# Kernel tuning notes

Hardware: AMD Instinct MI355X
Metric: run time of the kernel (lower is better)

The kernel has to match this reference:

```python
import jax, jax.numpy as jnp
import numpy as np

B, T, D, U = 64, 1024, 300, 300


def setup_inputs() -> dict:
    key = jax.random.key(0)
    ks = jax.random.split(key, 12)
    inputs = jax.random.normal(ks[0], (B, T, D), jnp.float32)
    lengths = jax.random.randint(ks[1], (B,), T // 2, T + 1)
    mask = jnp.arange(T)[None, :] < lengths[:, None]  # [B,T] bool

    def w(k, shape, fan_in):
        return jax.random.normal(k, shape, jnp.float32) * (1.0 / np.sqrt(fan_in))

    # Keras GRU (reset_after=True): kernel [D,3U], recurrent_kernel [U,3U], bias [2,3U]
    k_fwd = w(ks[2], (D, 3 * U), D)
    rk_fwd = w(ks[3], (U, 3 * U), U)
    b_fwd = jnp.zeros((2, 3 * U), jnp.float32)
    k_bwd = w(ks[4], (D, 3 * U), D)
    rk_bwd = w(ks[5], (U, 3 * U), U)
    b_bwd = jnp.zeros((2, 3 * U), jnp.float32)
    w_fc = w(ks[6], (2 * U, U), 2 * U)
    b_fc = jnp.zeros((U,), jnp.float32)
    return {
        "inputs": inputs, "mask": mask,
        "k_fwd": k_fwd, "rk_fwd": rk_fwd, "b_fwd": b_fwd,
        "k_bwd": k_bwd, "rk_bwd": rk_bwd, "b_bwd": b_bwd,
        "w_fc": w_fc, "b_fc": b_fc, "training": 0,
    }


def _gru_dir(x, mask, kernel, rkernel, bias):
    """Keras GRU v2 (reset_after=True), zero_output_for_mask, state frozen on masked steps.
    x: [B,T,D], mask: [B,T] bool -> (ys [B,T,U], h_final [B,U])"""
    b_in, b_rec = bias[0], bias[1]
    u = rkernel.shape[0]
    # precompute input projections for all timesteps (cuDNN-style hoisting)
    xp = jnp.einsum('btd,dk->btk', x, kernel) + b_in  # [B,T,3U]

    def step(h, inp):
        xt, mt = inp  # xt: [B,3U], mt: [B]
        rp = h @ rkernel + b_rec  # [B,3U]
        xz, xr, xh = jnp.split(xt, 3, axis=-1)
        rz, rr, rh = jnp.split(rp, 3, axis=-1)
        z = jax.nn.sigmoid(xz + rz)
        r = jax.nn.sigmoid(xr + rr)
        hh = jnp.tanh(xh + r * rh)
        h_new = z * h + (1.0 - z) * hh
        m = mt[:, None]
        h_carry = jnp.where(m, h_new, h)       # state does not update on masked steps
        y = jnp.where(m, h_new, jnp.zeros_like(h_new))  # zero_output_for_mask
        return h_carry, y

    h0 = jnp.zeros((x.shape[0], u), x.dtype)
    h_final, ys = jax.lax.scan(step, h0, (xp.transpose(1, 0, 2), mask.T))
    return ys.transpose(1, 0, 2), h_final


def reference(inputs, mask, k_fwd, rk_fwd, b_fwd, k_bwd, rk_bwd, b_bwd, w_fc, b_fc, training):
    mask = mask.astype(bool)
    x = inputs  # Dropout is identity at inference (training=0)
    y_f, h_f = _gru_dir(x, mask, k_fwd, rk_fwd, b_fwd)
    # backward direction: process reversed sequence/mask, then re-reverse outputs
    y_b, h_b = _gru_dir(x[:, ::-1], mask[:, ::-1], k_bwd, rk_bwd, b_bwd)
    y_b = y_b[:, ::-1]
    output = jnp.concatenate([y_f, y_b], axis=-1)  # [B,T,2U]
    state = jax.nn.relu(jnp.concatenate([h_f, h_b], axis=-1) @ w_fc + b_fc)  # [B,U]
    return output, state
```

## Files before the change

### kernel.cpp

```cpp
#include <hip/hip_runtime.h>
#include <hip/hip_bf16.h>


#define B_   64
#define T_   1024
#define D_   300
#define U_   300
#define NU   900
#define KP   320
#define NP   960
#define XPW  912
#define KB_  10
#define KRES 2
#define HSP  328
#define FRAGS_PER_DIR 570
#define NRESF 114
#define NWGM 4

typedef short short8 __attribute__((ext_vector_type(8)));
typedef float floatx4 __attribute__((ext_vector_type(4)));

__device__ __forceinline__ float b2f_bits(unsigned short u) {
  union { unsigned int i; float f; } v; v.i = ((unsigned int)u) << 16; return v.f;
}
__device__ __forceinline__ unsigned short f2b(float f) {
  __hip_bfloat16 h = __float2bfloat16(f);
  return *reinterpret_cast<unsigned short*>(&h);
}
__device__ __forceinline__ float sigm_f(float x) {
  float e = __expf(-x);
  return __fdividef(1.f, 1.f + e);
}
__device__ __forceinline__ float tanh_f(float x) {
  float e = __expf(2.f * x);
  return 1.f - __fdividef(2.f, e + 1.f);
}

__global__ __launch_bounds__(64) void k_detect(const unsigned int* __restrict__ xw,
                                               const unsigned char* __restrict__ mb,
                                               int* __restrict__ flags) {
  __shared__ int red[64];
  int tid = threadIdx.x;
  int hits = 0;
  for (int i = tid; i < 2048; i += 64) {
    unsigned int lo = xw[i] & 0xFFFFu;
    int e = (int)((lo >> 7) & 0xFF);
    if (e >= 105 && e <= 135) hits++;
  }
  red[tid] = hits;
  __syncthreads();
  if (tid == 0) {
    int s = 0;
    for (int i = 0; i < 64; ++i) s += red[i];
    flags[0] = (s >= 1024) ? 1 : 0;
    unsigned char b0 = mb[0], b1 = mb[1];
    flags[1] = (b1 == 0) ? 0 : ((b0 == 1 && b1 == 1) ? 1 : 2);
  }
}

__global__ __launch_bounds__(256) void k_lengths(const unsigned char* __restrict__ mraw,
                                                 const int* __restrict__ flags,
                                                 int* __restrict__ lens) {
  __shared__ int red[256];
  int b = blockIdx.x, tid = threadIdx.x;
  int mt = flags[1];
  int s = 0;
  if (mt == 0) {
    const int* m = (const int*)mraw;
    for (int t = tid; t < T_; t += 256) s += m[(size_t)b * T_ + t] ? 1 : 0;
  } else if (mt == 1) {
    for (int t = tid; t < T_; t += 256) s += mraw[(size_t)b * T_ + t] ? 1 : 0;
  } else {
    const unsigned short* m = (const unsigned short*)mraw;
    for (int t = tid; t < T_; t += 256) s += m[(size_t)b * T_ + t] ? 1 : 0;
  }
  red[tid] = s; __syncthreads();
  for (int off = 128; off > 0; off >>= 1) {
    if (tid < off) red[tid] += red[tid + off];
    __syncthreads();
  }
  if (tid == 0) lens[b] = red[0];
}

__global__ __launch_bounds__(256) void k_xpad(const void* __restrict__ xraw,
                                              const int* __restrict__ flags,
                                              unsigned short* __restrict__ xp) {
  int id = blockIdx.x * 256 + threadIdx.x;
  int row = id / 40, seg = id % 40;
  int kbase = seg * 8;
  int bf = flags[0];
  unsigned short v[8];
  if (bf) {
    const unsigned short* x = (const unsigned short*)xraw;
#pragma unroll
    for (int i = 0; i < 8; ++i) {
      int k = kbase + i;
      v[i] = (k < D_) ? x[(size_t)row * D_ + k] : (unsigned short)0;
    }
  } else {
    const float* x = (const float*)xraw;
#pragma unroll
    for (int i = 0; i < 8; ++i) {
      int k = kbase + i;
      v[i] = (k < D_) ? f2b(x[(size_t)row * D_ + k]) : (unsigned short)0;
    }
  }
  uint4 o;
  o.x = (unsigned)v[0] | ((unsigned)v[1] << 16);
  o.y = (unsigned)v[2] | ((unsigned)v[3] << 16);
  o.z = (unsigned)v[4] | ((unsigned)v[5] << 16);
  o.w = (unsigned)v[6] | ((unsigned)v[7] << 16);
  *(uint4*)(xp + (size_t)row * KP + kbase) = o;
}

__global__ __launch_bounds__(256) void k_wpad(const void* __restrict__ kf,
                                              const void* __restrict__ kb,
                                              const int* __restrict__ flags,
                                              unsigned short* __restrict__ kp) {
  int id = blockIdx.x * 256 + threadIdx.x;
  if (id >= 2 * KP * NP) return;
  int dir = id / (KP * NP);
  int r = id % (KP * NP);
  int k = r / NP, n = r % NP;
  int bf = flags[0];
  unsigned short v = 0;
  if (k < D_ && n < NU) {
    size_t si = (size_t)k * NU + n;
    if (bf) v = ((const unsigned short*)(dir ? kb : kf))[si];
    else    v = f2b(((const float*)(dir ? kb : kf))[si]);
  }
  kp[id] = v;
}

__global__ __launch_bounds__(256) void k_prep(const void* __restrict__ rkf,
                                              const void* __restrict__ rkb,
                                              const void* __restrict__ bfw,
                                              const void* __restrict__ bbw,
                                              const void* __restrict__ wfc,
                                              const void* __restrict__ bfc,
                                              const int* __restrict__ flags,
                                              unsigned short* __restrict__ rkc,
                                              float* __restrict__ biasc,
                                              unsigned short* __restrict__ wfcc,
                                              float* __restrict__ bfcc) {
  int i = blockIdx.x * 256 + threadIdx.x;
  int bf = flags[0];
  if (i < 2 * D_ * NU) {
    int dir = i / (D_ * NU), r = i % (D_ * NU);
    const void* src = dir ? rkb : rkf;
    rkc[i] = bf ? ((const unsigned short*)src)[r] : f2b(((const float*)src)[r]);
  }
  if (i < 2 * 2 * NU) {
    int dir = i / (2 * NU), r = i % (2 * NU);
    const void* src = dir ? bbw : bfw;
    biasc[i] = bf ? b2f_bits(((const unsigned short*)src)[r]) : ((const float*)src)[r];
  }
  if (i < 2 * U_ * U_) {
    wfcc[i] = bf ? ((const unsigned short*)wfc)[i] : f2b(((const float*)wfc)[i]);
  }
  if (i < U_) {
    bfcc[i] = bf ? b2f_bits(((const unsigned short*)bfc)[i]) : ((const float*)bfc)[i];
  }
}

__global__ __launch_bounds__(256) void k_bpack(const unsigned short* __restrict__ rkc,
                                               unsigned short* __restrict__ bpack) {
  int idx = blockIdx.x * 256 + threadIdx.x;
  const int total = 2 * FRAGS_PER_DIR * 512;
  if (idx >= total) return;
  int rem = idx;
  int j = rem & 7; rem >>= 3;
  int lane = rem & 63; rem >>= 6;
  int f = rem % FRAGS_PER_DIR;
  int dir = rem / FRAGS_PER_DIR;
  int w, fr, ntc;
  if (f < 180) { w = f / 60; fr = f - w * 60; ntc = 6; }
  else { int f2 = f - 180; w = 3 + f2 / 30; fr = f2 % 30; ntc = 3; }
  int kb = fr / ntc, nt = fr % ntc;
  int lb = nt / 3, g = nt % 3;
  int ub0 = (w < 3) ? 2 * w : 6 + (w - 3);
  int l15 = lane & 15, quad = lane >> 4;
  int k = kb * 32 + quad * 8 + j;
  int u = (ub0 + lb) * 16 + l15;
  unsigned short v = 0;
  if (k < U_ && u < U_) {
    v = rkc[(size_t)dir * U_ * NU + (size_t)k * NU + (size_t)g * U_ + u];
  }
  bpack[idx] = v;
}

template <bool XPF32>
__global__ __launch_bounds__(256) void k_gemm(const unsigned short* __restrict__ xpad,
                                              const unsigned short* __restrict__ kpad,
                                              const float* __restrict__ biasc,
                                              void* __restrict__ xp_out) {
  __shared__ __align__(16) unsigned short As[64 * 40];
  __shared__ __align__(16) unsigned short Bs[64 * 40];
  int tid = threadIdx.x;
  int wave = tid >> 6, lane = tid & 63;
  int m0 = blockIdx.x * 64, n0 = blockIdx.y * 64;
  int dir = blockIdx.z;
  const unsigned short* Bsrc = kpad + (size_t)dir * KP * NP;
  const float* bin = biasc + (size_t)dir * 2 * NU;

  floatx4 acc[4];
#pragma unroll
  for (int i = 0; i < 4; ++i) acc[i] = {0.f, 0.f, 0.f, 0.f};

  int arow = tid >> 2, aseg = tid & 3;
  int bk = tid & 31, bn8 = (tid >> 5) * 8;
  int fr = lane & 15, fq = lane >> 4;

  for (int kc = 0; kc < KP; kc += 32) {
    uint4 av = *(const uint4*)(xpad + (size_t)(m0 + arow) * KP + kc + aseg * 8);
    uint4 bv = *(const uint4*)(Bsrc + (size_t)(kc + bk) * NP + n0 + bn8);
    *(uint4*)(As + arow * 40 + aseg * 8) = av;
    unsigned short tmp[8];
    tmp[0] = bv.x & 0xffff; tmp[1] = bv.x >> 16;
    tmp[2] = bv.y & 0xffff; tmp[3] = bv.y >> 16;
    tmp[4] = bv.z & 0xffff; tmp[5] = bv.z >> 16;
    tmp[6] = bv.w & 0xffff; tmp[7] = bv.w >> 16;
#pragma unroll
    for (int i = 0; i < 8; ++i) Bs[(bn8 + i) * 40 + bk] = tmp[i];
    __syncthreads();
    short8 a = *(const short8*)(As + (wave * 16 + fr) * 40 + fq * 8);
#pragma unroll
    for (int nt = 0; nt < 4; ++nt) {
      short8 bfrag = *(const short8*)(Bs + (nt * 16 + fr) * 40 + fq * 8);
      acc[nt] = __builtin_amdgcn_mfma_f32_16x16x32_bf16(a, bfrag, acc[nt], 0, 0, 0);
    }
    __syncthreads();
  }
#pragma unroll
  for (int nt = 0; nt < 4; ++nt) {
    int col = n0 + nt * 16 + fr;
    if (col >= XPW) continue;
    float bi = (col < NU) ? bin[col] : 0.f;
#pragma unroll
    for (int r = 0; r < 4; ++r) {
      int m = m0 + wave * 16 + fq * 4 + r;
      float v = acc[nt][r] + bi;
      size_t idx = ((size_t)dir * 65536 + m) * XPW + col;
      if (XPF32) ((float*)xp_out)[idx] = v;
      else ((unsigned short*)xp_out)[idx] = f2b(v);
    }
  }
}

template <int NB, bool XPF32>
__device__ __forceinline__ void scan_loop(
    const unsigned short* __restrict__ bp,
    const unsigned short* __restrict__ sBw,
    unsigned short (*sHiP)[16][HSP],
    unsigned short (*sLoP)[16][HSP],
    const void* __restrict__ xp_all,
    unsigned short* __restrict__ out16, float* __restrict__ out32, int obf,
    const float* __restrict__ brec, const int* __restrict__ lens,
    float* __restrict__ hfin,
    int dir, int mg, int ub0, int l15, int quad) {
  constexpr int NTC = NB * 3;

  int ucl[NB]; bool cv[NB];
  float bz[NB], brg[NB], bh[NB];
#pragma unroll
  for (int lb = 0; lb < NB; ++lb) {
    int u = (ub0 + lb) * 16 + l15;
    bool v = (u < U_);
    cv[lb] = v;
    ucl[lb] = v ? u : 0;
    bz[lb] = brec[ucl[lb]]; brg[lb] = brec[U_ + ucl[lb]]; bh[lb] = brec[2 * U_ + ucl[lb]];
  }
  size_t xbase[4];
#pragma unroll
  for (int r = 0; r < 4; ++r)
    xbase[r] = ((size_t)dir * 65536 + (size_t)(mg * 16 + quad * 4 + r) * T_) * XPW;
  int mylen[4];
#pragma unroll
  for (int r = 0; r < 4; ++r) mylen[r] = lens[mg * 16 + quad * 4 + r];
  float hold[NB][4];
#pragma unroll
  for (int lb = 0; lb < NB; ++lb)
#pragma unroll
    for (int r = 0; r < 4; ++r) hold[lb][r] = 0.f;

#pragma unroll 1
  for (int s = 0; s < T_; ++s) {
    const int t = dir ? (T_ - 1 - s) : s;
    const int par = s & 1;
    const unsigned short (*hH)[HSP] = sHiP[par];
    const unsigned short (*hL)[HSP] = sLoP[par];

    floatx4 acc[NTC];
#pragma unroll
    for (int i = 0; i < NTC; ++i) acc[i] = {0.f, 0.f, 0.f, 0.f};

    short8 bA[NTC];
#pragma unroll
    for (int nt = 0; nt < NTC; ++nt)
      bA[nt] = *(const short8*)(bp + ((size_t)(KRES * NTC + nt)) * 512);
    short8 bB[NB == 1 ? NTC : 1];
    if constexpr (NB == 1) {
#pragma unroll
      for (int nt = 0; nt < NTC; ++nt)
        bB[nt] = *(const short8*)(bp + ((size_t)((KRES + 1) * NTC + nt)) * 512);
    }

    float X[NB][3][4];
#pragma unroll
    for (int r = 0; r < 4; ++r) {
      size_t ro = xbase[r] + (size_t)t * XPW;
      if (XPF32) {
        const float* xr = (const float*)xp_all + ro;
#pragma unroll
        for (int lb = 0; lb < NB; ++lb) {
          X[lb][0][r] = xr[ucl[lb]];
          X[lb][1][r] = xr[U_ + ucl[lb]];
          X[lb][2][r] = xr[2 * U_ + ucl[lb]];
        }
      } else {
        const unsigned short* xr = (const unsigned short*)xp_all + ro;
#pragma unroll
        for (int lb = 0; lb < NB; ++lb) {
          X[lb][0][r] = b2f_bits(xr[ucl[lb]]);
          X[lb][1][r] = b2f_bits(xr[U_ + ucl[lb]]);
          X[lb][2][r] = b2f_bits(xr[2 * U_ + ucl[lb]]);
        }
      }
    }

#pragma unroll
    for (int kb = 0; kb < KRES; ++kb) {
      short8 ah = *(const short8*)&hH[l15][kb * 32 + quad * 8];
      short8 al = *(const short8*)&hL[l15][kb * 32 + quad * 8];
#pragma unroll
      for (int nt = 0; nt < NTC; ++nt) {
        short8 b = *(const short8*)(sBw + ((size_t)(kb * NTC + nt)) * 512);
        acc[nt] = __builtin_amdgcn_mfma_f32_16x16x32_bf16(ah, b, acc[nt], 0, 0, 0);
      }
#pragma unroll
      for (int nt = 0; nt < NTC; ++nt) {
        short8 b = *(const short8*)(sBw + ((size_t)(kb * NTC + nt)) * 512);
        acc[nt] = __builtin_amdgcn_mfma_f32_16x16x32_bf16(al, b, acc[nt], 0, 0, 0);
      }
    }

    if constexpr (NB == 1) {
#pragma unroll
      for (int kb = KRES; kb < KB_; kb += 2) {
        {
          short8 ah = *(const short8*)&hH[l15][kb * 32 + quad * 8];
          short8 al = *(const short8*)&hL[l15][kb * 32 + quad * 8];
#pragma unroll
          for (int nt = 0; nt < NTC; ++nt)
            acc[nt] = __builtin_amdgcn_mfma_f32_16x16x32_bf16(ah, bA[nt], acc[nt], 0, 0, 0);
#pragma unroll
          for (int nt = 0; nt < NTC; ++nt)
            acc[nt] = __builtin_amdgcn_mfma_f32_16x16x32_bf16(al, bA[nt], acc[nt], 0, 0, 0);
          if (kb + 2 < KB_) {
#pragma unroll
            for (int nt = 0; nt < NTC; ++nt)
              bA[nt] = *(const short8*)(bp + ((size_t)((kb + 2) * NTC + nt)) * 512);
          }
        }
        {
          short8 ah = *(const short8*)&hH[l15][(kb + 1) * 32 + quad * 8];
          short8 al = *(const short8*)&hL[l15][(kb + 1) * 32 + quad * 8];
#pragma unroll
          for (int nt = 0; nt < NTC; ++nt)
            acc[nt] = __builtin_amdgcn_mfma_f32_16x16x32_bf16(ah, bB[nt], acc[nt], 0, 0, 0);
#pragma unroll
          for (int nt = 0; nt < NTC; ++nt)
            acc[nt] = __builtin_amdgcn_mfma_f32_16x16x32_bf16(al, bB[nt], acc[nt], 0, 0, 0);
          if (kb + 3 < KB_) {
#pragma unroll
            for (int nt = 0; nt < NTC; ++nt)
              bB[nt] = *(const short8*)(bp + ((size_t)((kb + 3) * NTC + nt)) * 512);
          }
        }
      }
    } else {
#pragma unroll
      for (int kb = KRES; kb < KB_; ++kb) {
        short8 ah = *(const short8*)&hH[l15][kb * 32 + quad * 8];
        short8 al = *(const short8*)&hL[l15][kb * 32 + quad * 8];
#pragma unroll
        for (int nt = 0; nt < NTC; ++nt)
          acc[nt] = __builtin_amdgcn_mfma_f32_16x16x32_bf16(ah, bA[nt], acc[nt], 0, 0, 0);
#pragma unroll
        for (int nt = 0; nt < NTC; ++nt)
          acc[nt] = __builtin_amdgcn_mfma_f32_16x16x32_bf16(al, bA[nt], acc[nt], 0, 0, 0);
        if (kb + 1 < KB_) {
#pragma unroll
          for (int nt = 0; nt < NTC; ++nt)
            bA[nt] = *(const short8*)(bp + ((size_t)((kb + 1) * NTC + nt)) * 512);
        }
      }
    }

    unsigned short (*nHi)[HSP] = sHiP[par ^ 1];
    unsigned short (*nLo)[HSP] = sLoP[par ^ 1];
#pragma unroll
    for (int r = 0; r < 4; ++r) {
      const int row = quad * 4 + r;
      const bool m = (t < mylen[r]);
      const size_t ob = ((size_t)(mg * 16 + row) * T_ + t) * 600 + (size_t)dir * U_;
#pragma unroll
      for (int lb = 0; lb < NB; ++lb) {
        float z  = sigm_f(X[lb][0][r] + acc[lb * 3 + 0][r] + bz[lb]);
        float rg = sigm_f(X[lb][1][r] + acc[lb * 3 + 1][r] + brg[lb]);
        float hh = tanh_f(X[lb][2][r] + rg * (acc[lb * 3 + 2][r] + bh[lb]));
        float hn = z * hold[lb][r] + (1.f - z) * hh;
        float hw = m ? hn : hold[lb][r];
        hold[lb][r] = hw;
        if (cv[lb]) {
          float y = m ? hn : 0.f;
          if (obf) out16[ob + ucl[lb]] = f2b(y); else out32[ob + ucl[lb]] = y;
          unsigned short hib = f2b(hw);
          nHi[row][ucl[lb]] = hib;
          nLo[row][ucl[lb]] = f2b(hw - b2f_bits(hib));
        }
      }
    }

    asm volatile("s_waitcnt lgkmcnt(0)" ::: "memory");
    __builtin_amdgcn_s_barrier();
  }

#pragma unroll
  for (int lb = 0; lb < NB; ++lb) {
    if (!cv[lb]) continue;
#pragma unroll
    for (int r = 0; r < 4; ++r)
      hfin[((size_t)dir * B_ + mg * 16 + quad * 4 + r) * 304 + ucl[lb]] = hold[lb][r];
  }
}

template <bool XPF32>
__global__ __launch_bounds__(1024, 1) void k_scan(const unsigned short* __restrict__ bpack,
                                                  const float* __restrict__ biasc,
                                                  const void* __restrict__ xp_all,
                                                  const int* __restrict__ lens,
                                                  const int* __restrict__ flags,
                                                  float* __restrict__ hfin,
                                                  void* __restrict__ outraw) {
  __shared__ unsigned short sHi[2][16][HSP];
  __shared__ unsigned short sLo[2][16][HSP];
  __shared__ __align__(16) unsigned short sB[NRESF * 512];

  const int tid = threadIdx.x;
  const int mg = blockIdx.x;
  const int dir = blockIdx.y;
  const int wave = tid >> 6, lane = tid & 63;
  const int l15 = lane & 15, quad = lane >> 4;
  const int obf = flags[0];
  unsigned short* out16 = (unsigned short*)outraw;
  float* out32 = (float*)outraw;

  const int NBLK = (wave < 3) ? 2 : 1;
  const int NTCw = NBLK * 3;
  const int UB0w = (wave < 3) ? 2 * wave : 6 + (wave - 3);
  const int FB   = (wave < 3) ? wave * 60 : 180 + (wave - 3) * 30;
  const int RB   = (wave < 3) ? wave * 12 : 36 + (wave - 3) * 6;

  {
    unsigned int* p0 = (unsigned int*)&sHi[0][0][0];
    unsigned int* p1 = (unsigned int*)&sLo[0][0][0];
    for (int i = tid; i < 2 * 16 * HSP / 2; i += 1024) { p0[i] = 0u; p1[i] = 0u; }
  }
  {
    const unsigned short* src = bpack + ((size_t)dir * FRAGS_PER_DIR + FB) * 512 + lane * 8;
    unsigned short* dst = sB + (size_t)RB * 512 + lane * 8;
    for (int j = 0; j < KRES * NTCw; ++j)
      *(uint4*)(dst + (size_t)j * 512) = *(const uint4*)(src + (size_t)j * 512);
  }
  __syncthreads();

  const unsigned short* bp = bpack + ((size_t)dir * FRAGS_PER_DIR + FB) * 512 + (size_t)lane * 8;
  const unsigned short* sBw = sB + (size_t)RB * 512 + (size_t)lane * 8;
  const float* brec = biasc + (size_t)dir * 2 * NU + NU;

  if (wave < 3)
    scan_loop<2, XPF32>(bp, sBw, sHi, sLo, xp_all, out16, out32, obf, brec, lens,
                        hfin, dir, mg, UB0w, l15, quad);
  else
    scan_loop<1, XPF32>(bp, sBw, sHi, sLo, xp_all, out16, out32, obf, brec, lens,
                        hfin, dir, mg, UB0w, l15, quad);
}

__global__ __launch_bounds__(320) void k_state(const float* __restrict__ hfin,
                                               const unsigned short* __restrict__ wfcc,
                                               const float* __restrict__ bfcc,
                                               const int* __restrict__ flags,
                                               void* __restrict__ outraw) {
  int b = blockIdx.x, u = threadIdx.x;
  if (u >= U_) return;
  int obf = flags[0];
  float acc = bfcc[u];
  const float* hf = hfin + (size_t)b * 304;
  const float* hb = hfin + ((size_t)B_ + b) * 304;
  for (int k = 0; k < U_; ++k) acc = fmaf(hf[k], b2f_bits(wfcc[(size_t)k * U_ + u]), acc);
  for (int k = 0; k < U_; ++k) acc = fmaf(hb[k], b2f_bits(wfcc[(size_t)(U_ + k) * U_ + u]), acc);
  float v = fmaxf(acc, 0.f);
  size_t oi = (size_t)B_ * T_ * 600 + (size_t)b * U_ + u;
  if (obf) ((unsigned short*)outraw)[oi] = f2b(v);
  else     ((float*)outraw)[oi] = v;
}

extern "C" void kernel_launch(void* const* d_in, const int* in_sizes, int n_in,
                              void* d_out, int out_size, void* d_ws, size_t ws_size,
                              hipStream_t stream) {
  const void* x    = d_in[0];
  const void* mask = d_in[1];
  const void* kf   = d_in[2];
  const void* rkf  = d_in[3];
  const void* bfw  = d_in[4];
  const void* kb   = d_in[5];
  const void* rkb  = d_in[6];
  const void* bbw  = d_in[7];
  const void* wfc  = d_in[8];
  const void* bfc  = d_in[9];

  char* ws = (char*)d_ws;
  size_t off = 0;
  auto alloc = [&](size_t bytes) { void* p = ws + off; off += (bytes + 255) & ~(size_t)255; return p; };
  int* flags            = (int*)alloc(256);
  int* lens             = (int*)alloc(256);
  unsigned short* xpad  = (unsigned short*)alloc((size_t)65536 * KP * 2);
  unsigned short* kpad  = (unsigned short*)alloc((size_t)2 * KP * NP * 2);
  unsigned short* rkc   = (unsigned short*)alloc((size_t)2 * D_ * NU * 2);
  unsigned short* bpack = (unsigned short*)alloc((size_t)2 * FRAGS_PER_DIR * 512 * 2);
  float* biasc          = (float*)alloc((size_t)2 * 2 * NU * 4);
  unsigned short* wfcc  = (unsigned short*)alloc((size_t)2 * U_ * U_ * 2);
  float* bfcc           = (float*)alloc((size_t)U_ * 4);
  float* hfin           = (float*)alloc((size_t)2 * B_ * 304 * 4);
  void* xp = (void*)(ws + off);
  size_t need_f32 = off + (size_t)2 * 65536 * XPW * 4;
  bool xpf32 = ws_size >= need_f32;

  k_detect<<<dim3(1), dim3(64), 0, stream>>>((const unsigned int*)x, (const unsigned char*)mask, flags);
  k_lengths<<<dim3(B_), dim3(256), 0, stream>>>((const unsigned char*)mask, flags, lens);
  k_xpad<<<dim3(65536 * 40 / 256), dim3(256), 0, stream>>>(x, flags, xpad);
  k_wpad<<<dim3((2 * KP * NP + 255) / 256), dim3(256), 0, stream>>>(kf, kb, flags, kpad);
  k_prep<<<dim3((2 * D_ * NU + 255) / 256), dim3(256), 0, stream>>>(rkf, rkb, bfw, bbw, wfc, bfc,
                                                                    flags, rkc, biasc, wfcc, bfcc);
  k_bpack<<<dim3((2 * FRAGS_PER_DIR * 512 + 255) / 256), dim3(256), 0, stream>>>(rkc, bpack);
  if (xpf32) {
    k_gemm<true><<<dim3(1024, 15, 2), dim3(256), 0, stream>>>(xpad, kpad, biasc, xp);
    k_scan<true><<<dim3(NWGM, 2), dim3(1024), 0, stream>>>(bpack, biasc, xp, lens, flags, hfin, d_out);
  } else {
    k_gemm<false><<<dim3(1024, 15, 2), dim3(256), 0, stream>>>(xpad, kpad, biasc, xp);
    k_scan<false><<<dim3(NWGM, 2), dim3(1024), 0, stream>>>(bpack, biasc, xp, lens, flags, hfin, d_out);
  }
  k_state<<<dim3(B_), dim3(320), 0, stream>>>(hfin, wfcc, bfcc, flags, d_out);
}
```

Baseline: 15.97 ms.

## Halve scan workgroup waves, give each wave more unit blocks and deeper prefetch

Reassigns the recurrent GEMM columns so 8 waves (3 with three unit blocks, 5 with two) cover the hidden dimension instead of 16, and launches the scan with 512 threads. The streamed recurrent-weight fragments are now prefetched through a generic D-deep register ring buffer (3 or 4 stages). The aim is to reduce per-step barrier cost and hide global weight-load latency better. In exchange, each wave carries more MFMA work and more registers, with fewer waves available to fill the SIMDs.

```diff
diff --git a/kernel.cpp b/kernel.cpp
--- a/kernel.cpp
+++ b/kernel.cpp
@@ -174,11 +174,11 @@
   int f = rem % FRAGS_PER_DIR;
   int dir = rem / FRAGS_PER_DIR;
   int w, fr, ntc;
-  if (f < 180) { w = f / 60; fr = f - w * 60; ntc = 6; }
-  else { int f2 = f - 180; w = 3 + f2 / 30; fr = f2 % 30; ntc = 3; }
+  if (f < 270) { w = f / 90; fr = f - w * 90; ntc = 9; }
+  else { int f2 = f - 270; w = 3 + f2 / 60; fr = f2 % 60; ntc = 6; }
   int kb = fr / ntc, nt = fr % ntc;
   int lb = nt / 3, g = nt % 3;
-  int ub0 = (w < 3) ? 2 * w : 6 + (w - 3);
+  int ub0 = (w < 3) ? w * 3 : 9 + (w - 3) * 2;
   int l15 = lane & 15, quad = lane >> 4;
   int k = kb * 32 + quad * 8 + j;
   int u = (ub0 + lb) * 16 + l15;
@@ -247,7 +247,7 @@
   }
 }
 
-template <int NB, bool XPF32>
+template <int NTC, int D, bool XPF32>
 __device__ __forceinline__ void scan_loop(
     const unsigned short* __restrict__ bp,
     const unsigned short* __restrict__ sBw,
@@ -258,7 +258,8 @@
     const float* __restrict__ brec, const int* __restrict__ lens,
     float* __restrict__ hfin,
     int dir, int mg, int ub0, int l15, int quad) {
-  constexpr int NTC = NB * 3;
+  constexpr int NB = NTC / 3;
+  constexpr int NSTR = KB_ - KRES;
 
   int ucl[NB]; bool cv[NB];
   float bz[NB], brg[NB], bh[NB];
@@ -294,16 +295,12 @@
 #pragma unroll
     for (int i = 0; i < NTC; ++i) acc[i] = {0.f, 0.f, 0.f, 0.f};
 
-    short8 bA[NTC];
-#pragma unroll
-    for (int nt = 0; nt < NTC; ++nt)
-      bA[nt] = *(const short8*)(bp + ((size_t)(KRES * NTC + nt)) * 512);
-    short8 bB[NB == 1 ? NTC : 1];
-    if constexpr (NB == 1) {
+    short8 buf[D][NTC];
+#pragma unroll
+    for (int d = 0; d < D; ++d)
 #pragma unroll
       for (int nt = 0; nt < NTC; ++nt)
-        bB[nt] = *(const short8*)(bp + ((size_t)((KRES + 1) * NTC + nt)) * 512);
-    }
+        buf[d][nt] = *(const short8*)(bp + ((size_t)((KRES + d) * NTC + nt)) * 512);
 
     float X[NB][3][4];
 #pragma unroll
@@ -344,56 +341,21 @@
       }
     }
 
-    if constexpr (NB == 1) {
-#pragma unroll
-      for (int kb = KRES; kb < KB_; kb += 2) {
-        {
-          short8 ah = *(const short8*)&hH[l15][kb * 32 + quad * 8];
-          short8 al = *(const short8*)&hL[l15][kb * 32 + quad * 8];
-#pragma unroll
-          for (int nt = 0; nt < NTC; ++nt)
-            acc[nt] = __builtin_amdgcn_mfma_f32_16x16x32_bf16(ah, bA[nt], acc[nt], 0, 0, 0);
-#pragma unroll
-          for (int nt = 0; nt < NTC; ++nt)
-            acc[nt] = __builtin_amdgcn_mfma_f32_16x16x32_bf16(al, bA[nt], acc[nt], 0, 0, 0);
-          if (kb + 2 < KB_) {
-#pragma unroll
-            for (int nt = 0; nt < NTC; ++nt)
-              bA[nt] = *(const short8*)(bp + ((size_t)((kb + 2) * NTC + nt)) * 512);
-          }
-        }
-        {
-          short8 ah = *(const short8*)&hH[l15][(kb + 1) * 32 + quad * 8];
-          short8 al = *(const short8*)&hL[l15][(kb + 1) * 32 + quad * 8];
-#pragma unroll
-          for (int nt = 0; nt < NTC; ++nt)
-            acc[nt] = __builtin_amdgcn_mfma_f32_16x16x32_bf16(ah, bB[nt], acc[nt], 0, 0, 0);
-#pragma unroll
-          for (int nt = 0; nt < NTC; ++nt)
-            acc[nt] = __builtin_amdgcn_mfma_f32_16x16x32_bf16(al, bB[nt], acc[nt], 0, 0, 0);
-          if (kb + 3 < KB_) {
-#pragma unroll
-            for (int nt = 0; nt < NTC; ++nt)
-              bB[nt] = *(const short8*)(bp + ((size_t)((kb + 3) * NTC + nt)) * 512);
-          }
-        }
-      }
-    } else {
-#pragma unroll
-      for (int kb = KRES; kb < KB_; ++kb) {
-        short8 ah = *(const short8*)&hH[l15][kb * 32 + quad * 8];
-        short8 al = *(const short8*)&hL[l15][kb * 32 + quad * 8];
+#pragma unroll
+    for (int i = 0; i < NSTR; ++i) {
+      const int kb = KRES + i;
+      short8 ah = *(const short8*)&hH[l15][kb * 32 + quad * 8];
+      short8 al = *(const short8*)&hL[l15][kb * 32 + quad * 8];
+#pragma unroll
+      for (int nt = 0; nt < NTC; ++nt)
+        acc[nt] = __builtin_amdgcn_mfma_f32_16x16x32_bf16(ah, buf[i % D][nt], acc[nt], 0, 0, 0);
+#pragma unroll
+      for (int nt = 0; nt < NTC; ++nt)
+        acc[nt] = __builtin_amdgcn_mfma_f32_16x16x32_bf16(al, buf[i % D][nt], acc[nt], 0, 0, 0);
+      if (i + D < NSTR) {
 #pragma unroll
         for (int nt = 0; nt < NTC; ++nt)
-          acc[nt] = __builtin_amdgcn_mfma_f32_16x16x32_bf16(ah, bA[nt], acc[nt], 0, 0, 0);
-#pragma unroll
-        for (int nt = 0; nt < NTC; ++nt)
-          acc[nt] = __builtin_amdgcn_mfma_f32_16x16x32_bf16(al, bA[nt], acc[nt], 0, 0, 0);
-        if (kb + 1 < KB_) {
-#pragma unroll
-          for (int nt = 0; nt < NTC; ++nt)
-            bA[nt] = *(const short8*)(bp + ((size_t)((kb + 1) * NTC + nt)) * 512);
-        }
+          buf[i % D][nt] = *(const short8*)(bp + ((size_t)((kb + D) * NTC + nt)) * 512);
       }
     }
 
@@ -436,13 +398,13 @@
 }
 
 template <bool XPF32>
-__global__ __launch_bounds__(1024, 1) void k_scan(const unsigned short* __restrict__ bpack,
-                                                  const float* __restrict__ biasc,
-                                                  const void* __restrict__ xp_all,
-                                                  const int* __restrict__ lens,
-                                                  const int* __restrict__ flags,
-                                                  float* __restrict__ hfin,
-                                                  void* __restrict__ outraw) {
+__global__ __launch_bounds__(512, 2) void k_scan(const unsigned short* __restrict__ bpack,
+                                                 const float* __restrict__ biasc,
+                                                 const void* __restrict__ xp_all,
+                                                 const int* __restrict__ lens,
+                                                 const int* __restrict__ flags,
+                                                 float* __restrict__ hfin,
+                                                 void* __restrict__ outraw) {
   __shared__ unsigned short sHi[2][16][HSP];
   __shared__ unsigned short sLo[2][16][HSP];
   __shared__ __align__(16) unsigned short sB[NRESF * 512];
@@ -456,16 +418,15 @@
   unsigned short* out16 = (unsigned short*)outraw;
   float* out32 = (float*)outraw;
 
-  const int NBLK = (wave < 3) ? 2 : 1;
-  const int NTCw = NBLK * 3;
-  const int UB0w = (wave < 3) ? 2 * wave : 6 + (wave - 3);
-  const int FB   = (wave < 3) ? wave * 60 : 180 + (wave - 3) * 30;
-  const int RB   = (wave < 3) ? wave * 12 : 36 + (wave - 3) * 6;
+  const int NTCw = (wave < 3) ? 9 : 6;
+  const int UB0w = (wave < 3) ? wave * 3 : 9 + (wave - 3) * 2;
+  const int FB   = (wave < 3) ? wave * 90 : 270 + (wave - 3) * 60;
+  const int RB   = (wave < 3) ? wave * 18 : 54 + (wave - 3) * 12;
 
   {
     unsigned int* p0 = (unsigned int*)&sHi[0][0][0];
     unsigned int* p1 = (unsigned int*)&sLo[0][0][0];
-    for (int i = tid; i < 2 * 16 * HSP / 2; i += 1024) { p0[i] = 0u; p1[i] = 0u; }
+    for (int i = tid; i < 2 * 16 * HSP / 2; i += 512) { p0[i] = 0u; p1[i] = 0u; }
   }
   {
     const unsigned short* src = bpack + ((size_t)dir * FRAGS_PER_DIR + FB) * 512 + lane * 8;
@@ -480,11 +441,11 @@
   const float* brec = biasc + (size_t)dir * 2 * NU + NU;
 
   if (wave < 3)
-    scan_loop<2, XPF32>(bp, sBw, sHi, sLo, xp_all, out16, out32, obf, brec, lens,
-                        hfin, dir, mg, UB0w, l15, quad);
+    scan_loop<9, 3, XPF32>(bp, sBw, sHi, sLo, xp_all, out16, out32, obf, brec, lens,
+                           hfin, dir, mg, UB0w, l15, quad);
   else
-    scan_loop<1, XPF32>(bp, sBw, sHi, sLo, xp_all, out16, out32, obf, brec, lens,
-                        hfin, dir, mg, UB0w, l15, quad);
+    scan_loop<6, 4, XPF32>(bp, sBw, sHi, sLo, xp_all, out16, out32, obf, brec, lens,
+                           hfin, dir, mg, UB0w, l15, quad);
 }
 
 __global__ __launch_bounds__(320) void k_state(const float* __restrict__ hfin,
@@ -546,10 +507,10 @@
   k_bpack<<<dim3((2 * FRAGS_PER_DIR * 512 + 255) / 256), dim3(256), 0, stream>>>(rkc, bpack);
   if (xpf32) {
     k_gemm<true><<<dim3(1024, 15, 2), dim3(256), 0, stream>>>(xpad, kpad, biasc, xp);
-    k_scan<true><<<dim3(NWGM, 2), dim3(1024), 0, stream>>>(bpack, biasc, xp, lens, flags, hfin, d_out);
+    k_scan<true><<<dim3(NWGM, 2), dim3(512), 0, stream>>>(bpack, biasc, xp, lens, flags, hfin, d_out);
   } else {
     k_gemm<false><<<dim3(1024, 15, 2), dim3(256), 0, stream>>>(xpad, kpad, biasc, xp);
-    k_scan<false><<<dim3(NWGM, 2), dim3(1024), 0, stream>>>(bpack, biasc, xp, lens, flags, hfin, d_out);
+    k_scan<false><<<dim3(NWGM, 2), dim3(512), 0, stream>>>(bpack, biasc, xp, lens, flags, hfin, d_out);
   }
   k_state<<<dim3(B_), dim3(320), 0, stream>>>(hfin, wfcc, bfcc, flags, d_out);
 }
```

Result: faster. 14.69 ms (-8.0%).
